# Kernel tuning notes

Hardware: AMD Instinct MI355X
Metric: run time of the kernel (lower is better)

The kernel has to match this reference:

```python
import jax, jax.numpy as jnp
import numpy as np

N_NODES = 100
F_IN = 65536
C_OUT = 60
ACTION_DIM = 100
N_EDGES = 2000


def setup_inputs() -> dict:
    key = jax.random.key(0)
    ks = jax.random.split(key, 16)
    s = 0.02
    return {
        "substrate_features": jax.random.normal(ks[0], (1, N_NODES, F_IN), jnp.float32),
        "edge_index": jax.random.randint(ks[1], (2, N_EDGES), 0, N_NODES, dtype=jnp.int32),
        "v_cpu_demand_t": jax.random.uniform(ks[2], (1,), jnp.float32),
        "v_bw_demand_t": jax.random.uniform(ks[3], (1,), jnp.float32),
        "num_pending_v_nodes_t": jax.random.uniform(ks[4], (1,), jnp.float32),
        "actor_w": jax.random.normal(ks[5], (3, F_IN, C_OUT), jnp.float32) * s,
        "actor_b": jax.random.normal(ks[6], (C_OUT,), jnp.float32) * s,
        "critic_w": jax.random.normal(ks[7], (3, F_IN, C_OUT), jnp.float32) * s,
        "critic_b": jax.random.normal(ks[8], (C_OUT,), jnp.float32) * s,
        "actor_fc_w": jax.random.normal(ks[9], (N_NODES * C_OUT + 3, ACTION_DIM), jnp.float32) * s,
        "actor_fc_b": jax.random.normal(ks[10], (ACTION_DIM,), jnp.float32) * s,
        "critic_fc_w": jax.random.normal(ks[11], (N_NODES * C_OUT + 3, 1), jnp.float32) * s,
        "critic_fc_b": jax.random.normal(ks[12], (1,), jnp.float32) * s,
    }


def cheb_conv(x, edge_index, W, b):
    # ChebConv, K=3, sym normalization, lambda_max=2 (PyG defaults).
    # With lambda_max=2 the scaled Laplacian is L_hat = -D^{-1/2} A D^{-1/2}
    # (diagonal becomes 0 after the -1 self-loop shift).
    # x: [1, N, F]; edge_index: [2, E]; W: [3, F, C]; b: [C]
    src, dst = edge_index[0], edge_index[1]
    n = x.shape[1]
    deg = jax.ops.segment_sum(jnp.ones(src.shape[0], x.dtype), src, num_segments=n)
    dis = jnp.where(deg > 0, jax.lax.rsqrt(jnp.where(deg > 0, deg, 1.0)), 0.0)
    norm = -(dis[src] * dis[dst])  # [E], L_hat off-diagonal entries
    x2 = x[0]  # [N, F]

    def prop(z):  # z: [N, F] -> L_hat @ z via gather/scatter over edges
        return jax.ops.segment_sum(z[src] * norm[:, None], dst, num_segments=n)

    Tx0 = x2
    Tx1 = prop(Tx0)
    Tx2 = 2.0 * prop(Tx1) - Tx0
    out = Tx0 @ W[0] + Tx1 @ W[1] + Tx2 @ W[2] + b  # [N, C]
    return out[None]  # [1, N, C]


def reference(substrate_features, edge_index, v_cpu_demand_t, v_bw_demand_t,
              num_pending_v_nodes_t, actor_w, actor_b, critic_w, critic_b,
              actor_fc_w, actor_fc_b, critic_fc_w, critic_fc_b):
    emb_a = jnp.tanh(cheb_conv(substrate_features, edge_index, actor_w, actor_b))
    emb_a = emb_a.reshape(1, -1)  # [1, N*60]
    emb_c = jnp.tanh(cheb_conv(substrate_features, edge_index, critic_w, critic_b))
    emb_c = emb_c.reshape(1, -1)
    extras = [v_cpu_demand_t[None], v_bw_demand_t[None], num_pending_v_nodes_t[None]]  # each [1,1]
    state_a = jnp.concatenate([emb_a] + extras, axis=1)  # [1, 6003]
    state_c = jnp.concatenate([emb_c] + extras, axis=1)
    logits = state_a @ actor_fc_w + actor_fc_b  # [1, action_dim]
    values = state_c @ critic_fc_w + critic_fc_b  # [1, 1]
    return (logits, values)
```

## Files before the change

### kernel.cpp

```cpp
#include <hip/hip_runtime.h>
#include <stdint.h>

#define F_IN 65536
#define NN 100
#define CO 60
#define G_SPLIT 128
#define KC (F_IN/G_SPLIT)
#define BK 64
#define NIT (KC/BK)
#define AST 72

typedef short v8s __attribute__((ext_vector_type(8)));
typedef float v4f __attribute__((ext_vector_type(4)));

__device__ __forceinline__ unsigned int f2bf(float x){
  unsigned int u = __float_as_uint(x);
  u += 0x7fffu + ((u>>16)&1u);
  return u>>16;
}

__device__ __forceinline__ v4f mfma16(v8s a, v8s b, v4f c){
  return __builtin_amdgcn_mfma_f32_16x16x32_bf16(a,b,c,0,0,0);
}

__global__ __launch_bounds__(256,2)
void k_gemm(const float* __restrict__ x, const float* __restrict__ aw,
            const float* __restrict__ cw, float* __restrict__ dst, int partial){
  const int s  = blockIdx.x;
  const int g  = blockIdx.y;
  const int k0 = s*KC;
  const int tid = threadIdx.x;
  const int wave = tid>>6, lane = tid&63, quad = lane>>4, nl = lane&15;
  const int c0 = wave*16;
  const int ccl = min(c0+nl, CO-1);

  const float* W  = (g<3) ? (aw + (size_t)g*F_IN*CO) : (cw + (size_t)(g-3)*F_IN*CO);
  const float* wp = W + (size_t)(k0 + quad*8)*CO + ccl;

  __shared__ __align__(16) unsigned short Al[2][112*AST];

  float4 ra[7];
  float  rb[16];
  #pragma unroll
  for(int p=0;p<7;++p){
    int lin = p*256 + tid, row = lin>>4, q = lin&15;
    int rcl = min(row, NN-1);
    ra[p] = *(const float4*)(x + (size_t)rcl*F_IN + k0 + q*4);
  }
  #pragma unroll
  for(int u=0;u<16;++u) rb[u] = wp[((u>>3)*32 + (u&7))*CO];

  v4f acc[7];
  #pragma unroll
  for(int i=0;i<7;++i){ v4f z={0.f,0.f,0.f,0.f}; acc[i]=z; }

  for(int it=0; it<NIT; ++it){
    unsigned short* buf = Al[it&1];
    #pragma unroll
    for(int p=0;p<7;++p){
      int lin = p*256 + tid, row = lin>>4, q = lin&15;
      uint2 w;
      w.x = f2bf(ra[p].x) | (f2bf(ra[p].y)<<16);
      w.y = f2bf(ra[p].z) | (f2bf(ra[p].w)<<16);
      *(uint2*)(buf + row*AST + q*4) = w;
    }
    v8s fB0, fB1;
    #pragma unroll
    for(int j=0;j<8;++j){
      fB0[j] = (short)f2bf(rb[j]);
      fB1[j] = (short)f2bf(rb[8+j]);
    }
    __syncthreads();
    if(it+1 < NIT){
      const int kb = k0 + (it+1)*BK;
      #pragma unroll
      for(int p=0;p<7;++p){
        int lin = p*256 + tid, row = lin>>4, q = lin&15;
        int rcl = min(row, NN-1);
        ra[p] = *(const float4*)(x + (size_t)rcl*F_IN + kb + q*4);
      }
      #pragma unroll
      for(int u=0;u<16;++u) rb[u] = wp[((it+1)*BK + (u>>3)*32 + (u&7))*CO];
    }
    #pragma unroll
    for(int mt=0; mt<7; ++mt){
      const unsigned short* arow = buf + (mt*16+nl)*AST + quad*8;
      v8s a0 = *(const v8s*)(arow);
      v8s a1 = *(const v8s*)(arow+32);
      acc[mt] = mfma16(a0, fB0, acc[mt]);
      acc[mt] = mfma16(a1, fB1, acc[mt]);
    }
  }

  const int c = c0 + nl;
  if(c < CO){
    if(partial){
      float* pd = dst + ((size_t)g*G_SPLIT + s)*(NN*CO);
      #pragma unroll
      for(int mt=0;mt<7;++mt){
        #pragma unroll
        for(int i=0;i<4;++i){
          int m = mt*16 + quad*4 + i;
          if(m < NN) pd[m*CO + c] = acc[mt][i];
        }
      }
    } else {
      float* pd = dst + (size_t)g*(NN*CO);
      #pragma unroll
      for(int mt=0;mt<7;++mt){
        #pragma unroll
        for(int i=0;i<4;++i){
          int m = mt*16 + quad*4 + i;
          if(m < NN) atomicAdd(pd + m*CO + c, acc[mt][i]);
        }
      }
    }
  }
}

__global__ void k_reduce(const float* __restrict__ P, float* __restrict__ Y){
  int o = blockIdx.x*256 + threadIdx.x;
  if(o >= 6*NN*CO) return;
  int gg = o/(NN*CO), r = o - gg*(NN*CO);
  const float* p = P + (size_t)gg*G_SPLIT*(NN*CO) + (size_t)blockIdx.y*32*(NN*CO) + r;
  float a0=0.f,a1=0.f,a2=0.f,a3=0.f;
  #pragma unroll 2
  for(int s4=0;s4<32;s4+=4){
    a0 += p[(s4  )*(NN*CO)];
    a1 += p[(s4+1)*(NN*CO)];
    a2 += p[(s4+2)*(NN*CO)];
    a3 += p[(s4+3)*(NN*CO)];
  }
  atomicAdd(&Y[o], (a0+a1)+(a2+a3));
}

__global__ void k_cheb(const float* __restrict__ Y, const int* __restrict__ ei,
                       const float* __restrict__ ab, const float* __restrict__ cb,
                       float* __restrict__ emb){
  const int net = blockIdx.x / CO;
  const int c   = blockIdx.x % CO;
  const int t   = threadIdx.x;
  __shared__ float L[NN][NN+1];
  __shared__ float dis[NN];
  __shared__ int   deg[NN];
  __shared__ float y0[NN], y1[NN], y2[NN], zu[NN];

  for(int i=t;i<NN*(NN+1);i+=128) ((float*)L)[i]=0.f;
  if(t<NN) deg[t]=0;
  __syncthreads();
  for(int e=t;e<2000;e+=128) atomicAdd(&deg[ei[e]],1);
  __syncthreads();
  if(t<NN) dis[t] = deg[t]>0 ? rsqrtf((float)deg[t]) : 0.f;
  __syncthreads();
  for(int e=t;e<2000;e+=128){
    int s = ei[e], d = ei[2000+e];
    atomicAdd(&L[d][s], -dis[s]*dis[d]);
  }
  if(t<NN){
    const float* yb = Y + (size_t)net*3*NN*CO + t*CO + c;
    y0[t]=yb[0]; y1[t]=yb[NN*CO]; y2[t]=yb[2*NN*CO];
  }
  __syncthreads();
  if(t<NN){
    float s=0.f;
    #pragma unroll 4
    for(int j=0;j<NN;++j) s += L[t][j]*y2[j];
    zu[t] = y1[t] + 2.f*s;
  }
  __syncthreads();
  if(t<NN){
    float s=0.f;
    #pragma unroll 4
    for(int j=0;j<NN;++j) s += L[t][j]*zu[j];
    float b = (net==0) ? ab[c] : cb[c];
    emb[net*NN*CO + t*CO + c] = tanhf(y0[t] - y2[t] + s + b);
  }
}

#define FCB 25
__global__ void k_fc(const float* __restrict__ emb, const float* __restrict__ afw,
                     const float* __restrict__ afb, const float* __restrict__ cfw,
                     const float* __restrict__ cfb, const float* __restrict__ s0,
                     const float* __restrict__ s1, const float* __restrict__ s2,
                     float* __restrict__ out){
  const int b = blockIdx.x;
  const int t = threadIdx.x;
  if(b < FCB){
    const int jj = t & 127, half = t >> 7;
    if(jj < 100){
      const int i0 = b*240 + half*120;
      const float* w = afw + (size_t)i0*100 + jj;
      const float* e = emb + i0;
      float p = 0.f;
      #pragma unroll 4
      for(int i=0;i<120;++i) p += e[i]*w[(size_t)i*100];
      atomicAdd(&out[jj], p);
    }
  } else {
    float p = 0.f;
    const float* e = emb + 6000;
    for(int i=t;i<6000;i+=256) p += e[i]*cfw[i];
    #pragma unroll
    for(int o=32;o>0;o>>=1) p += __shfl_down(p,o,64);
    __shared__ float red[4];
    if((t&63)==0) red[t>>6]=p;
    __syncthreads();
    if(t==0){
      float tot = red[0]+red[1]+red[2]+red[3];
      out[100] = tot + s0[0]*cfw[6000] + s1[0]*cfw[6001] + s2[0]*cfw[6002] + cfb[0];
    }
    if(t<100){
      atomicAdd(&out[t], afb[t] + s0[0]*afw[600000+t] + s1[0]*afw[600100+t] + s2[0]*afw[600200+t]);
    }
  }
}

extern "C" void kernel_launch(void* const* d_in, const int* in_sizes, int n_in,
                              void* d_out, int out_size, void* d_ws, size_t ws_size,
                              hipStream_t stream){
  const float* x   = (const float*)d_in[0];
  const int*   ei  = (const int*)d_in[1];
  const float* s0  = (const float*)d_in[2];
  const float* s1  = (const float*)d_in[3];
  const float* s2  = (const float*)d_in[4];
  const float* aw  = (const float*)d_in[5];
  const float* ab  = (const float*)d_in[6];
  const float* cw  = (const float*)d_in[7];
  const float* cb  = (const float*)d_in[8];
  const float* afw = (const float*)d_in[9];
  const float* afb = (const float*)d_in[10];
  const float* cfw = (const float*)d_in[11];
  const float* cfb = (const float*)d_in[12];
  float* out = (float*)d_out;

  float* Y   = (float*)d_ws;
  float* emb = Y + 6*NN*CO;
  float* P   = emb + 2*NN*CO;
  const size_t need = (size_t)(6*NN*CO + 2*NN*CO + (size_t)6*G_SPLIT*NN*CO)*sizeof(float);
  const int partial = (ws_size >= need) ? 1 : 0;

  hipMemsetAsync(Y, 0, 6*NN*CO*sizeof(float), stream);
  hipMemsetAsync(out, 0, 101*sizeof(float), stream);

  k_gemm<<<dim3(G_SPLIT,6), 256, 0, stream>>>(x, aw, cw, partial ? P : Y, partial);
  if(partial){
    k_reduce<<<dim3((6*NN*CO+255)/256, 4), 256, 0, stream>>>(P, Y);
  }
  k_cheb<<<120, 128, 0, stream>>>(Y, ei, ab, cb, emb);
  k_fc<<<FCB+1, 256, 0, stream>>>(emb, afw, afb, cfw, cfb, s0, s1, s2, out);
}
```

Before: 212.4 us.

## Pre-convert features to bf16 and stream GEMM tiles via async global-to-LDS copies

Adds a separate kernel that converts the input features to bf16 once into workspace. The GEMM then streams A and W tiles directly into double-buffered LDS with global_load_lds instead of staging them through registers, and uses an XOR-swizzled A layout to avoid bank conflicts. The aim is to halve the A-operand bytes read by the six GEMM groups, which each re-read x, and to free registers and overlap loads with MFMA work. The cost is an extra kernel pass over x (read fp32, write bf16), about 13 MB more workspace, and W still converted from fp32 out of LDS on every iteration.

```diff
diff --git a/kernel.cpp b/kernel.cpp
--- a/kernel.cpp
+++ b/kernel.cpp
@@ -8,7 +8,6 @@
 #define KC (F_IN/G_SPLIT)
 #define BK 64
 #define NIT (KC/BK)
-#define AST 72
 
 typedef short v8s __attribute__((ext_vector_type(8)));
 typedef float v4f __attribute__((ext_vector_type(4)));
@@ -18,75 +17,90 @@
   u += 0x7fffu + ((u>>16)&1u);
   return u>>16;
 }
-
 __device__ __forceinline__ v4f mfma16(v8s a, v8s b, v4f c){
   return __builtin_amdgcn_mfma_f32_16x16x32_bf16(a,b,c,0,0,0);
 }
+__device__ __forceinline__ void cp16(const void* g, void* l){
+  __builtin_amdgcn_global_load_lds((const __attribute__((address_space(1))) void*)g,
+                                   (__attribute__((address_space(3))) void*)l, 16, 0, 0);
+}
+
+__global__ __launch_bounds__(256)
+void k_cvt(const float* __restrict__ x, unsigned short* __restrict__ xb){
+  int i = blockIdx.x*256 + threadIdx.x;
+  float4 v = ((const float4*)x)[i];
+  uint2 w;
+  w.x = f2bf(v.x) | (f2bf(v.y)<<16);
+  w.y = f2bf(v.z) | (f2bf(v.w)<<16);
+  ((uint2*)xb)[i] = w;
+}
 
 __global__ __launch_bounds__(256,2)
-void k_gemm(const float* __restrict__ x, const float* __restrict__ aw,
+void k_gemm(const unsigned short* __restrict__ xb, const float* __restrict__ aw,
             const float* __restrict__ cw, float* __restrict__ dst, int partial){
-  const int s  = blockIdx.x;
-  const int g  = blockIdx.y;
+  const int s = blockIdx.x, g = blockIdx.y;
   const int k0 = s*KC;
-  const int tid = threadIdx.x;
-  const int wave = tid>>6, lane = tid&63, quad = lane>>4, nl = lane&15;
-  const int c0 = wave*16;
-  const int ccl = min(c0+nl, CO-1);
-
-  const float* W  = (g<3) ? (aw + (size_t)g*F_IN*CO) : (cw + (size_t)(g-3)*F_IN*CO);
-  const float* wp = W + (size_t)(k0 + quad*8)*CO + ccl;
-
-  __shared__ __align__(16) unsigned short Al[2][112*AST];
-
-  float4 ra[7];
-  float  rb[16];
-  #pragma unroll
-  for(int p=0;p<7;++p){
-    int lin = p*256 + tid, row = lin>>4, q = lin&15;
+  const int tid = threadIdx.x, wave = tid>>6, lane = tid&63, quad = lane>>4, nl = lane&15;
+  const int c0 = wave*16, ccl = min(c0+nl, CO-1);
+
+  __shared__ __align__(16) unsigned short Ab[2][112*64];
+  __shared__ __align__(16) float          Wb[2][BK*CO];
+
+  const float* W = (g<3) ? (aw + (size_t)g*F_IN*CO) : (cw + (size_t)(g-3)*F_IN*CO);
+
+  const int nA = (wave<2) ? 4 : 3;
+  const int nW = (wave<3) ? 4 : 3;
+  const unsigned short* ag[4];
+  unsigned int aoff[4];
+  #pragma unroll
+  for(int ti=0; ti<4; ++ti){
+    int t   = wave + 4*ti;
+    int row = 8*t + (lane>>3);
     int rcl = min(row, NN-1);
-    ra[p] = *(const float4*)(x + (size_t)rcl*F_IN + k0 + q*4);
-  }
-  #pragma unroll
-  for(int u=0;u<16;++u) rb[u] = wp[((u>>3)*32 + (u&7))*CO];
+    int lch = (lane&7) ^ (row&7);
+    ag[ti]  = xb + (size_t)rcl*F_IN + k0 + lch*8;
+    aoff[ti] = t*512 + lane*8;
+  }
+  const float* wg[4];
+  unsigned int woff[4];
+  #pragma unroll
+  for(int ti=0; ti<4; ++ti){
+    int t = wave + 4*ti;
+    wg[ti]   = W + (size_t)k0*CO + t*256 + lane*4;
+    woff[ti] = t*256 + lane*4;
+  }
 
   v4f acc[7];
   #pragma unroll
   for(int i=0;i<7;++i){ v4f z={0.f,0.f,0.f,0.f}; acc[i]=z; }
 
+  #pragma unroll
+  for(int ti=0; ti<4; ++ti) if(ti<nA) cp16(ag[ti], &Ab[0][aoff[ti]]);
+  #pragma unroll
+  for(int ti=0; ti<4; ++ti) if(ti<nW) cp16(wg[ti], &Wb[0][woff[ti]]);
+
   for(int it=0; it<NIT; ++it){
-    unsigned short* buf = Al[it&1];
-    #pragma unroll
-    for(int p=0;p<7;++p){
-      int lin = p*256 + tid, row = lin>>4, q = lin&15;
-      uint2 w;
-      w.x = f2bf(ra[p].x) | (f2bf(ra[p].y)<<16);
-      w.y = f2bf(ra[p].z) | (f2bf(ra[p].w)<<16);
-      *(uint2*)(buf + row*AST + q*4) = w;
+    __syncthreads();
+    const int b = it&1;
+    if(it+1 < NIT){
+      const int nb = (it+1)&1;
+      #pragma unroll
+      for(int ti=0; ti<4; ++ti) if(ti<nA) cp16(ag[ti] + (it+1)*BK, &Ab[nb][aoff[ti]]);
+      #pragma unroll
+      for(int ti=0; ti<4; ++ti) if(ti<nW) cp16(wg[ti] + (size_t)(it+1)*BK*CO, &Wb[nb][woff[ti]]);
     }
     v8s fB0, fB1;
     #pragma unroll
     for(int j=0;j<8;++j){
-      fB0[j] = (short)f2bf(rb[j]);
-      fB1[j] = (short)f2bf(rb[8+j]);
-    }
-    __syncthreads();
-    if(it+1 < NIT){
-      const int kb = k0 + (it+1)*BK;
-      #pragma unroll
-      for(int p=0;p<7;++p){
-        int lin = p*256 + tid, row = lin>>4, q = lin&15;
-        int rcl = min(row, NN-1);
-        ra[p] = *(const float4*)(x + (size_t)rcl*F_IN + kb + q*4);
-      }
-      #pragma unroll
-      for(int u=0;u<16;++u) rb[u] = wp[((it+1)*BK + (u>>3)*32 + (u&7))*CO];
+      fB0[j] = (short)f2bf(Wb[b][(   quad*8+j)*CO + ccl]);
+      fB1[j] = (short)f2bf(Wb[b][(32+quad*8+j)*CO + ccl]);
     }
     #pragma unroll
     for(int mt=0; mt<7; ++mt){
-      const unsigned short* arow = buf + (mt*16+nl)*AST + quad*8;
-      v8s a0 = *(const v8s*)(arow);
-      v8s a1 = *(const v8s*)(arow+32);
+      int r  = mt*16 + nl;
+      int p0 = ((quad ^ (r&7))*8);
+      v8s a0 = *(const v8s*)&Ab[b][r*64 + p0];
+      v8s a1 = *(const v8s*)&Ab[b][r*64 + (p0^32)];
       acc[mt] = mfma16(a0, fB0, acc[mt]);
       acc[mt] = mfma16(a1, fB1, acc[mt]);
     }
@@ -233,16 +247,18 @@
   const float* cfb = (const float*)d_in[12];
   float* out = (float*)d_out;
 
-  float* Y   = (float*)d_ws;
+  unsigned short* xb = (unsigned short*)d_ws;
+  float* Y   = (float*)((char*)d_ws + 13107200);
   float* emb = Y + 6*NN*CO;
   float* P   = emb + 2*NN*CO;
-  const size_t need = (size_t)(6*NN*CO + 2*NN*CO + (size_t)6*G_SPLIT*NN*CO)*sizeof(float);
-  const int partial = (ws_size >= need) ? 1 : 0;
+  const size_t need_full = 13107200u + (size_t)(6*NN*CO + 2*NN*CO)*4 + (size_t)6*G_SPLIT*NN*CO*4;
+  const int partial = (ws_size >= need_full) ? 1 : 0;
 
   hipMemsetAsync(Y, 0, 6*NN*CO*sizeof(float), stream);
   hipMemsetAsync(out, 0, 101*sizeof(float), stream);
 
-  k_gemm<<<dim3(G_SPLIT,6), 256, 0, stream>>>(x, aw, cw, partial ? P : Y, partial);
+  k_cvt<<<6400, 256, 0, stream>>>(x, xb);
+  k_gemm<<<dim3(G_SPLIT,6), 256, 0, stream>>>(xb, aw, cw, partial ? P : Y, partial);
   if(partial){
     k_reduce<<<dim3((6*NN*CO+255)/256, 4), 256, 0, stream>>>(P, Y);
   }
```

New measurement: 216.3 us. Within noise of the previous version (+1.8%).
